# Performance work log

Hardware: AMD Instinct MI355X
Metric: run time of the kernel (lower is better)

Reference implementation:

```python
import jax, jax.numpy as jnp
import numpy as np

DIM = 768
NUM_HEADS = 12
HEAD_DIM = DIM // NUM_HEADS
SCALE = HEAD_DIM ** -0.5


def setup_inputs() -> dict:
    key = jax.random.key(0)
    k1, k2, k3, k4 = jax.random.split(key, 4)
    B, N = 4, 2048
    x = jax.random.normal(k1, (B, N, DIM), dtype=jnp.float32)
    w_qkv = jax.random.normal(k2, (DIM, 3 * DIM), dtype=jnp.float32) * (DIM ** -0.5)
    w_proj = jax.random.normal(k3, (DIM, DIM), dtype=jnp.float32) * (DIM ** -0.5)
    b_proj = jax.random.normal(k4, (DIM,), dtype=jnp.float32) * 0.02
    return {"x": x, "w_qkv": w_qkv, "w_proj": w_proj, "b_proj": b_proj}


def reference(x, w_qkv, w_proj, b_proj):
    B, N, C = x.shape
    H, Dh = NUM_HEADS, HEAD_DIM
    # qkv: [B, N, 3, H, Dh] -> q,k,v each [B, H, N, Dh]
    qkv = (x @ w_qkv).reshape(B, N, 3, H, Dh)
    q = qkv[:, :, 0].transpose(0, 2, 1, 3) * SCALE
    k = qkv[:, :, 1].transpose(0, 2, 1, 3)
    v = qkv[:, :, 2].transpose(0, 2, 1, 3)
    attn = jax.nn.softmax(jnp.einsum('bhnd,bhmd->bhnm', q, k), axis=-1)
    out = jnp.einsum('bhnm,bhmd->bhnd', attn, v)  # [B, H, N, Dh]
    out = out.transpose(0, 2, 1, 3).reshape(B, N, C)
    return out @ w_proj + b_proj
```

## Files before the change

kernel.cpp:

```cpp
#include <hip/hip_runtime.h>

typedef unsigned short u16;
typedef __bf16 bf16x8 __attribute__((ext_vector_type(8)));
typedef __bf16 bf16x4 __attribute__((ext_vector_type(4)));
typedef short s16x4 __attribute__((ext_vector_type(4)));
typedef float f32x4 __attribute__((ext_vector_type(4)));
typedef _Float16 f16x4 __attribute__((ext_vector_type(4)));
typedef unsigned short u16x8 __attribute__((ext_vector_type(8)));
typedef unsigned short u16x4 __attribute__((ext_vector_type(4)));

__device__ __forceinline__ u16 f2bf(float x) {
  union { float f; unsigned u; } c; c.f = x;
  unsigned r = c.u + 0x7FFFu + ((c.u >> 16) & 1u);
  return (u16)(r >> 16);
}

__device__ __forceinline__ void glds16(const void* g, void* s) {
  __builtin_amdgcn_global_load_lds(
      (const __attribute__((address_space(1))) unsigned int*)g,
      (__attribute__((address_space(3))) unsigned int*)s, 16, 0, 0);
}

__global__ __launch_bounds__(256) void k_pre(const float* __restrict__ x,
                                             u16* __restrict__ xbf,
                                             const float* __restrict__ wq,
                                             u16* __restrict__ wqt,
                                             const float* __restrict__ wp,
                                             u16* __restrict__ wpt) {
  __shared__ float tile[64 * 68];
  int bx = blockIdx.x;
  int tid = threadIdx.x;
  if (bx < 3072) {
    int i = bx * 256 + tid;
    const f32x4* xp = (const f32x4*)x + (size_t)i * 2;
    f32x4 a = xp[0], b = xp[1];
    u16x8 r;
    r[0] = f2bf(a[0]); r[1] = f2bf(a[1]); r[2] = f2bf(a[2]); r[3] = f2bf(a[3]);
    r[4] = f2bf(b[0]); r[5] = f2bf(b[1]); r[6] = f2bf(b[2]); r[7] = f2bf(b[3]);
    *((u16x8*)xbf + i) = r;
    return;
  }
  const float* src; u16* dst; int Nn, n0, k0;
  const int K = 768;
  if (bx < 3504) { int b2 = bx - 3072; src = wq; dst = wqt; Nn = 2304;
                   n0 = (b2 % 36) * 64; k0 = (b2 / 36) * 64; }
  else           { int b2 = bx - 3504; src = wp; dst = wpt; Nn = 768;
                   n0 = (b2 % 12) * 64; k0 = (b2 / 12) * 64; }
  int rr = tid >> 4, cc = tid & 15;
#pragma unroll
  for (int r = 0; r < 4; ++r) {
    int k = r * 16 + rr;
    f32x4 v = *(const f32x4*)(src + (size_t)(k0 + k) * Nn + n0 + cc * 4);
    *(f32x4*)(tile + k * 68 + cc * 4) = v;
  }
  __syncthreads();
#pragma unroll
  for (int r = 0; r < 4; ++r) {
    int n = r * 16 + rr;
    u16x4 o;
#pragma unroll
    for (int j = 0; j < 4; ++j) o[j] = f2bf(tile[(cc * 4 + j) * 68 + n]);
    *(u16x4*)(dst + (size_t)(n0 + n) * K + k0 + cc * 4) = o;
  }
}

template <int BM, int N, bool PROJ>
__global__ __launch_bounds__(256) void k_gemm(const u16* __restrict__ A,
                                              const u16* __restrict__ Bt,
                                              u16* __restrict__ Co,
                                              float* __restrict__ Cf,
                                              const float* __restrict__ bias,
                                              u16* __restrict__ vt) {
  const int K = 768;
  const int FI = BM / 32;
  __shared__ u16 lA[BM * 64];
  __shared__ u16 lB[128 * 64];
  const int tid = threadIdx.x;
  const int wave = tid >> 6, lane = tid & 63;
  const int lr = lane & 15, lq = lane >> 4;
  const int m0 = blockIdx.x * BM, n0 = blockIdx.y * 128;
  const int wr = (wave >> 1) * (BM / 2), wc = (wave & 1) * 64;
  f32x4 acc[FI][4] = {};
  for (int k0 = 0; k0 < K; k0 += 64) {
#pragma unroll
    for (int r = 0; r < BM / 32; ++r) {
      int ch = r * 256 + tid;
      int mm = ch >> 3, cs = ch & 7;
      glds16(A + (size_t)(m0 + mm) * K + k0 + ((cs ^ (mm & 7)) << 3), lA + ch * 8);
    }
#pragma unroll
    for (int r = 0; r < 4; ++r) {
      int ch = r * 256 + tid;
      int mm = ch >> 3, cs = ch & 7;
      glds16(Bt + (size_t)(n0 + mm) * K + k0 + ((cs ^ (mm & 7)) << 3), lB + ch * 8);
    }
    __syncthreads();
#pragma unroll
    for (int ks = 0; ks < 2; ++ks) {
      bf16x8 af[FI], bfr[4];
#pragma unroll
      for (int f = 0; f < FI; ++f) {
        int ma = wr + f * 16 + lr;
        af[f] = *(const bf16x8*)(lA + (ma * 8 + ((ks * 4 + lq) ^ (ma & 7))) * 8);
      }
#pragma unroll
      for (int f = 0; f < 4; ++f) {
        int nb = wc + f * 16 + lr;
        bfr[f] = *(const bf16x8*)(lB + (nb * 8 + ((ks * 4 + lq) ^ (nb & 7))) * 8);
      }
#pragma unroll
      for (int fi = 0; fi < FI; ++fi)
#pragma unroll
        for (int fj = 0; fj < 4; ++fj)
          acc[fi][fj] = __builtin_amdgcn_mfma_f32_16x16x32_bf16(
              af[fi], bfr[fj], acc[fi][fj], 0, 0, 0);
    }
    __syncthreads();
  }
#pragma unroll
  for (int fi = 0; fi < FI; ++fi) {
#pragma unroll
    for (int fj = 0; fj < 4; ++fj) {
      int row = m0 + wr + fi * 16 + lq * 4;
      int col = n0 + wc + fj * 16 + lr;
      if constexpr (PROJ) {
        float bv = bias[col];
#pragma unroll
        for (int g = 0; g < 4; ++g)
          Cf[(size_t)(row + g) * N + col] = acc[fi][fj][g] + bv;
      } else {
        if (n0 + wc >= 1536) {
          int hh = (col - 1536) >> 6, dd = col & 63;
          u16x4 o;
#pragma unroll
          for (int g = 0; g < 4; ++g) o[g] = f2bf(acc[fi][fj][g]);
          *(u16x4*)(vt + (((size_t)(row >> 11) * 12 + hh) * 64 + dd) * 2048 +
                    (row & 2047)) = o;
        } else {
          const float qs = 0.18033688011112042f;
          float s = (col < 768) ? qs : 1.0f;
#pragma unroll
          for (int g = 0; g < 4; ++g)
            Co[(size_t)(row + g) * N + col] = f2bf(acc[fi][fj][g] * s);
        }
      }
    }
  }
}

__global__ __launch_bounds__(256, 4) void k_attn(const u16* __restrict__ qkv,
                                                 const u16* __restrict__ vt,
                                                 u16* __restrict__ p0,
                                                 u16* __restrict__ p1,
                                                 float* __restrict__ Lp) {
  const int SEQ = 2048, C3 = 2304;
  __shared__ u16 lK[128 * 64];
  __shared__ u16 lV[64 * 128];
  const int tid = threadIdx.x;
  const int wave = tid >> 6, lane = tid & 63;
  const int lr = lane & 15, lq = lane >> 4;
  const int n0 = blockIdx.x * 128;
  const int bh = blockIdx.y;
  const int jh = blockIdx.z;
  const int b = bh / 12, h = bh % 12;
  const u16* qb = qkv + (size_t)b * SEQ * C3 + h * 64;
  const u16* kb = qb + 768;
  const u16* vb = vt + (size_t)bh * 64 * SEQ;

#pragma unroll
  for (int r = 0; r < 4; ++r) {
    int ch = r * 256 + tid;
    int mm = ch >> 3, cs = ch & 7;
    glds16(qb + (size_t)(n0 + mm) * C3 + ((cs ^ (mm & 7)) << 3), lK + ch * 8);
  }
  __syncthreads();
  bf16x8 qf[2][2];
#pragma unroll
  for (int rf = 0; rf < 2; ++rf) {
    int mq = wave * 32 + rf * 16 + lr;
#pragma unroll
    for (int ks = 0; ks < 2; ++ks)
      qf[rf][ks] = *(const bf16x8*)(lK + (mq * 8 + ((ks * 4 + lq) ^ (mq & 7))) * 8);
  }

  const f32x4 biasC = {-8.f, -8.f, -8.f, -8.f};
  const s16x4 onesA = {16256, 16256, 16256, 16256};
  f32x4 O[2][4] = {};
  f32x4 L5[2] = {};

  for (int tt = 0; tt < 8; ++tt) {
    int j0 = jh * 1024 + tt * 128;
    __syncthreads();
#pragma unroll
    for (int r = 0; r < 4; ++r) {
      int ch = r * 256 + tid;
      int mm = ch >> 3, cs = ch & 7;
      glds16(kb + (size_t)(j0 + mm) * C3 + ((cs ^ (mm & 7)) << 3), lK + ch * 8);
      int dd = ch >> 4, ct = ch & 15;
      glds16(vb + (size_t)dd * SEQ + j0 + ((ct ^ (dd & 7)) << 3), lV + ch * 8);
    }
    __syncthreads();

#pragma unroll
    for (int half = 0; half < 2; ++half) {
      f32x4 S[4][2];
#pragma unroll
      for (int cf = 0; cf < 4; ++cf) {
        int j = (half * 4 + cf) * 16 + lr;
        bf16x8 kf = *(const bf16x8*)(lK + (j * 8 + (lq ^ (j & 7))) * 8);
#pragma unroll
        for (int rf = 0; rf < 2; ++rf)
          S[cf][rf] = __builtin_amdgcn_mfma_f32_16x16x32_bf16(
              kf, qf[rf][0], biasC, 0, 0, 0);
      }
#pragma unroll
      for (int cf = 0; cf < 4; ++cf) {
        int j = (half * 4 + cf) * 16 + lr;
        bf16x8 kf = *(const bf16x8*)(lK + (j * 8 + ((4 + lq) ^ (j & 7))) * 8);
#pragma unroll
        for (int rf = 0; rf < 2; ++rf)
          S[cf][rf] = __builtin_amdgcn_mfma_f32_16x16x32_bf16(
              kf, qf[rf][1], S[cf][rf], 0, 0, 0);
      }
      union PU { bf16x4 b; s16x4 s; } P[4][2];
#pragma unroll
      for (int cf = 0; cf < 4; ++cf)
#pragma unroll
        for (int rf = 0; rf < 2; ++rf) {
          bf16x4 pb;
#pragma unroll
          for (int g = 0; g < 4; ++g)
            pb[g] = (__bf16)__builtin_amdgcn_exp2f(S[cf][rf][g]);
          P[cf][rf].b = pb;
        }
#pragma unroll
      for (int cf = 0; cf < 4; ++cf) {
        int c2 = (half * 4 + cf) * 2 + (lq >> 1);
#pragma unroll
        for (int rf = 0; rf < 2; ++rf)
          L5[rf] = __builtin_amdgcn_mfma_f32_16x16x16bf16_1k(
              onesA, P[cf][rf].s, L5[rf], 0, 0, 0);
#pragma unroll
        for (int df = 0; df < 4; ++df) {
          int d = df * 16 + lr;
          s16x4 vf = *(const s16x4*)(lV + d * 128 + ((c2 ^ (d & 7)) << 3) + (lq & 1) * 4);
#pragma unroll
          for (int rf = 0; rf < 2; ++rf)
            O[rf][df] = __builtin_amdgcn_mfma_f32_16x16x16bf16_1k(
                vf, P[cf][rf].s, O[rf][df], 0, 0, 0);
        }
      }
    }
  }

  u16* pd = jh ? p1 : p0;
  float* Lb = Lp + (size_t)(jh * 48 + bh) * 2048;
#pragma unroll
  for (int rf = 0; rf < 2; ++rf) {
    int rowl = n0 + wave * 32 + rf * 16 + lr;
    if (lq == 0) Lb[rowl] = L5[rf][0];
    size_t row = (size_t)b * SEQ + rowl;
#pragma unroll
    for (int df = 0; df < 4; ++df) {
      union { f16x4 h; u16x4 u; } o;
#pragma unroll
      for (int g = 0; g < 4; ++g) o.h[g] = (_Float16)O[rf][df][g];
      *(u16x4*)(pd + row * 768 + h * 64 + df * 16 + lq * 4) = o.u;
    }
  }
}

__global__ __launch_bounds__(256) void k_merge(const u16* __restrict__ p0,
                                               u16* __restrict__ p1,
                                               const float* __restrict__ Lp) {
  int t = blockIdx.x * 256 + threadIdx.x;
  int row = t / 192, c4 = (t % 192) * 4;
  int hh = c4 >> 6;
  int bh = (row >> 11) * 12 + hh, rowl = row & 2047;
  float l = Lp[(size_t)bh * 2048 + rowl] + Lp[(size_t)(48 + bh) * 2048 + rowl];
  float inv = 1.0f / l;
  size_t off = (size_t)row * 768 + c4;
  union { f16x4 h; u16x4 u; } a, bb;
  a.u = *(const u16x4*)(p0 + off);
  bb.u = *(const u16x4*)(p1 + off);
  u16x4 o;
#pragma unroll
  for (int g = 0; g < 4; ++g)
    o[g] = f2bf(((float)a.h[g] + (float)bb.h[g]) * inv);
  *(u16x4*)(p1 + off) = o;
}

extern "C" void kernel_launch(void* const* d_in, const int* in_sizes, int n_in,
                              void* d_out, int out_size, void* d_ws, size_t ws_size,
                              hipStream_t stream) {
  const float* x = (const float*)d_in[0];
  const float* w_qkv = (const float*)d_in[1];
  const float* w_proj = (const float*)d_in[2];
  const float* b_proj = (const float*)d_in[3];
  float* out = (float*)d_out;
  char* ws = (char*)d_ws;
  u16* x_bf    = (u16*)(ws);
  u16* wqkv_t  = (u16*)(ws + 12582912);
  u16* wproj_t = (u16*)(ws + 16121856);
  u16* qkv     = (u16*)(ws + 17301504);
  u16* vt      = (u16*)(ws + 55050240);
  u16* aout    = (u16*)(ws + 67633152);
  float* Lp    = (float*)wqkv_t;

  k_pre<<<3648, 256, 0, stream>>>(x, x_bf, w_qkv, wqkv_t, w_proj, wproj_t);
  k_gemm<128, 2304, false><<<dim3(64, 18), 256, 0, stream>>>(x_bf, wqkv_t, qkv,
                                                             nullptr, nullptr, vt);
  k_attn<<<dim3(16, 48, 2), 256, 0, stream>>>(qkv, vt, x_bf, aout, Lp);
  k_merge<<<6144, 256, 0, stream>>>(x_bf, aout, Lp);
  k_gemm<64, 768, true><<<dim3(128, 6), 256, 0, stream>>>(aout, wproj_t, nullptr,
                                                          out, b_proj, nullptr);
}
```

Baseline: 239.0 us.

## Double-buffer K/V tiles in attention kernel with async LDS prefetch

Doubles the LDS buffers for K and V so the next tile's global-to-LDS loads are issued before computing on the current tile. Raw s_barrier and s_waitcnt vmcnt(8) let the loads overlap with compute. It also merges the two half-tile passes into one pass over 8 column fragments. This costs twice the LDS and more registers, and launch bounds drop to 2 blocks per CU, so occupancy and latency hiding across waves may fall.

Result: faster. 233.6 us (-2.2%).

```diff
diff --git a/kernel.cpp b/kernel.cpp
--- a/kernel.cpp
+++ b/kernel.cpp
@@ -148,14 +148,14 @@
   }
 }
 
-__global__ __launch_bounds__(256, 4) void k_attn(const u16* __restrict__ qkv,
+__global__ __launch_bounds__(256, 2) void k_attn(const u16* __restrict__ qkv,
                                                  const u16* __restrict__ vt,
                                                  u16* __restrict__ p0,
                                                  u16* __restrict__ p1,
                                                  float* __restrict__ Lp) {
   const int SEQ = 2048, C3 = 2304;
-  __shared__ u16 lK[128 * 64];
-  __shared__ u16 lV[64 * 128];
+  __shared__ u16 lK[2][128 * 64];
+  __shared__ u16 lV[2][64 * 128];
   const int tid = threadIdx.x;
   const int wave = tid >> 6, lane = tid & 63;
   const int lr = lane & 15, lq = lane >> 4;
@@ -171,7 +171,7 @@
   for (int r = 0; r < 4; ++r) {
     int ch = r * 256 + tid;
     int mm = ch >> 3, cs = ch & 7;
-    glds16(qb + (size_t)(n0 + mm) * C3 + ((cs ^ (mm & 7)) << 3), lK + ch * 8);
+    glds16(qb + (size_t)(n0 + mm) * C3 + ((cs ^ (mm & 7)) << 3), lK[0] + ch * 8);
   }
   __syncthreads();
   bf16x8 qf[2][2];
@@ -180,75 +180,91 @@
     int mq = wave * 32 + rf * 16 + lr;
 #pragma unroll
     for (int ks = 0; ks < 2; ++ks)
-      qf[rf][ks] = *(const bf16x8*)(lK + (mq * 8 + ((ks * 4 + lq) ^ (mq & 7))) * 8);
-  }
+      qf[rf][ks] = *(const bf16x8*)(lK[0] + (mq * 8 + ((ks * 4 + lq) ^ (mq & 7))) * 8);
+  }
+  __syncthreads();
 
   const f32x4 biasC = {-8.f, -8.f, -8.f, -8.f};
   const s16x4 onesA = {16256, 16256, 16256, 16256};
   f32x4 O[2][4] = {};
   f32x4 L5[2] = {};
 
-  for (int tt = 0; tt < 8; ++tt) {
-    int j0 = jh * 1024 + tt * 128;
-    __syncthreads();
+  const int smm = tid >> 3, scs = tid & 7;
+  const int sdd = tid >> 4, sct = tid & 15;
+
+  auto stage = [&](int t, int buf) {
+    int j0 = jh * 1024 + t * 128;
 #pragma unroll
     for (int r = 0; r < 4; ++r) {
       int ch = r * 256 + tid;
-      int mm = ch >> 3, cs = ch & 7;
-      glds16(kb + (size_t)(j0 + mm) * C3 + ((cs ^ (mm & 7)) << 3), lK + ch * 8);
-      int dd = ch >> 4, ct = ch & 15;
-      glds16(vb + (size_t)dd * SEQ + j0 + ((ct ^ (dd & 7)) << 3), lV + ch * 8);
-    }
-    __syncthreads();
-
-#pragma unroll
-    for (int half = 0; half < 2; ++half) {
-      f32x4 S[4][2];
-#pragma unroll
-      for (int cf = 0; cf < 4; ++cf) {
-        int j = (half * 4 + cf) * 16 + lr;
-        bf16x8 kf = *(const bf16x8*)(lK + (j * 8 + (lq ^ (j & 7))) * 8);
+      int mm = (r << 5) + smm;
+      glds16(kb + (size_t)(j0 + mm) * C3 + ((scs ^ (mm & 7)) << 3),
+             lK[buf] + ch * 8);
+      int dd = (r << 4) + sdd;
+      glds16(vb + (size_t)dd * SEQ + j0 + ((sct ^ (dd & 7)) << 3),
+             lV[buf] + ch * 8);
+    }
+  };
+
+  stage(0, 0);
+  for (int t = 0; t < 8; ++t) {
+    const int cur = t & 1;
+    const u16* K_ = lK[cur];
+    const u16* V_ = lV[cur];
+    asm volatile("s_barrier" ::: "memory");
+    if (t < 7) {
+      stage(t + 1, cur ^ 1);
+      asm volatile("s_waitcnt vmcnt(8)" ::: "memory");
+    } else {
+      asm volatile("s_waitcnt vmcnt(0)" ::: "memory");
+    }
+    asm volatile("s_barrier" ::: "memory");
+
+    f32x4 S[8][2];
+#pragma unroll
+    for (int cf = 0; cf < 8; ++cf) {
+      int j = cf * 16 + lr;
+      bf16x8 kf = *(const bf16x8*)(K_ + (j * 8 + (lq ^ (j & 7))) * 8);
+#pragma unroll
+      for (int rf = 0; rf < 2; ++rf)
+        S[cf][rf] = __builtin_amdgcn_mfma_f32_16x16x32_bf16(
+            kf, qf[rf][0], biasC, 0, 0, 0);
+    }
+#pragma unroll
+    for (int cf = 0; cf < 8; ++cf) {
+      int j = cf * 16 + lr;
+      bf16x8 kf = *(const bf16x8*)(K_ + (j * 8 + ((4 + lq) ^ (j & 7))) * 8);
+#pragma unroll
+      for (int rf = 0; rf < 2; ++rf)
+        S[cf][rf] = __builtin_amdgcn_mfma_f32_16x16x32_bf16(
+            kf, qf[rf][1], S[cf][rf], 0, 0, 0);
+    }
+    union PU { bf16x4 b; s16x4 s; } P[8][2];
+#pragma unroll
+    for (int cf = 0; cf < 8; ++cf)
+#pragma unroll
+      for (int rf = 0; rf < 2; ++rf) {
+        bf16x4 pb;
+#pragma unroll
+        for (int g = 0; g < 4; ++g)
+          pb[g] = (__bf16)__builtin_amdgcn_exp2f(S[cf][rf][g]);
+        P[cf][rf].b = pb;
+      }
+#pragma unroll
+    for (int cf = 0; cf < 8; ++cf) {
+      int c2 = cf * 2 + (lq >> 1);
+#pragma unroll
+      for (int rf = 0; rf < 2; ++rf)
+        L5[rf] = __builtin_amdgcn_mfma_f32_16x16x16bf16_1k(
+            onesA, P[cf][rf].s, L5[rf], 0, 0, 0);
+#pragma unroll
+      for (int df = 0; df < 4; ++df) {
+        int d = df * 16 + lr;
+        s16x4 vf = *(const s16x4*)(V_ + d * 128 + ((c2 ^ (d & 7)) << 3) + (lq & 1) * 4);
 #pragma unroll
         for (int rf = 0; rf < 2; ++rf)
-          S[cf][rf] = __builtin_amdgcn_mfma_f32_16x16x32_bf16(
-              kf, qf[rf][0], biasC, 0, 0, 0);
-      }
-#pragma unroll
-      for (int cf = 0; cf < 4; ++cf) {
-        int j = (half * 4 + cf) * 16 + lr;
-        bf16x8 kf = *(const bf16x8*)(lK + (j * 8 + ((4 + lq) ^ (j & 7))) * 8);
-#pragma unroll
-        for (int rf = 0; rf < 2; ++rf)
-          S[cf][rf] = __builtin_amdgcn_mfma_f32_16x16x32_bf16(
-              kf, qf[rf][1], S[cf][rf], 0, 0, 0);
-      }
-      union PU { bf16x4 b; s16x4 s; } P[4][2];
-#pragma unroll
-      for (int cf = 0; cf < 4; ++cf)
-#pragma unroll
-        for (int rf = 0; rf < 2; ++rf) {
-          bf16x4 pb;
-#pragma unroll
-          for (int g = 0; g < 4; ++g)
-            pb[g] = (__bf16)__builtin_amdgcn_exp2f(S[cf][rf][g]);
-          P[cf][rf].b = pb;
-        }
-#pragma unroll
-      for (int cf = 0; cf < 4; ++cf) {
-        int c2 = (half * 4 + cf) * 2 + (lq >> 1);
-#pragma unroll
-        for (int rf = 0; rf < 2; ++rf)
-          L5[rf] = __builtin_amdgcn_mfma_f32_16x16x16bf16_1k(
-              onesA, P[cf][rf].s, L5[rf], 0, 0, 0);
-#pragma unroll
-        for (int df = 0; df < 4; ++df) {
-          int d = df * 16 + lr;
-          s16x4 vf = *(const s16x4*)(lV + d * 128 + ((c2 ^ (d & 7)) << 3) + (lq & 1) * 4);
-#pragma unroll
-          for (int rf = 0; rf < 2; ++rf)
-            O[rf][df] = __builtin_amdgcn_mfma_f32_16x16x16bf16_1k(
-                vf, P[cf][rf].s, O[rf][df], 0, 0, 0);
-        }
+          O[rf][df] = __builtin_amdgcn_mfma_f32_16x16x16bf16_1k(
+              vf, P[cf][rf].s, O[rf][df], 0, 0, 0);
       }
     }
   }
```
